# Performance work log

Hardware: AMD Instinct MI355X
Metric: run time of the kernel (lower is better)

Reference implementation:

```python
import jax, jax.numpy as jnp
import numpy as np

SEQ, BATCH, D, N = 256, 4, 512, 32768
TEMP = 0.5


def setup_inputs() -> dict:
    key = jax.random.key(0)
    ks = jax.random.split(key, 16)
    d = D
    # xavier_uniform with gain 1/sqrt(2) for square [d,d]: limit = gain*sqrt(6/(d+d))
    lim_t = (1.0 / np.sqrt(2.0)) * np.sqrt(6.0 / (d + d))
    lim_g1 = np.sqrt(6.0 / (2 * d + d))  # default kaiming-ish scale approximated by xavier
    lim_g2 = np.sqrt(6.0 / (d + 1))
    inp = {
        "q": jax.random.normal(ks[0], (SEQ, BATCH, D), dtype=jnp.float32),
        "prev_layer_output": jax.random.normal(ks[1], (SEQ, BATCH, D), dtype=jnp.float32),
        "Wq": jax.random.uniform(ks[2], (D, D), jnp.float32, -lim_t, lim_t),
        "bq": jnp.zeros((D,), jnp.float32),
        "Wk": jax.random.uniform(ks[3], (D, D), jnp.float32, -lim_t, lim_t),
        "bk": jnp.zeros((D,), jnp.float32),
        "Wv": jax.random.uniform(ks[4], (D, D), jnp.float32, -lim_t, lim_t),
        "bv": jnp.zeros((D,), jnp.float32),
        "Wg1": jax.random.uniform(ks[5], (D, 2 * D), jnp.float32, -lim_g1, lim_g1),
        "bg1": jnp.zeros((D,), jnp.float32),
        "Wg2": jax.random.uniform(ks[6], (1, D), jnp.float32, -lim_g2, lim_g2),
        "bg2": jnp.zeros((1,), jnp.float32),
        "dstore_k": jax.random.normal(ks[7], (N, D), dtype=jnp.float32),
        "dstore_v": jax.random.normal(ks[8], (N, D), dtype=jnp.float32),
    }
    return inp


def reference(q, prev_layer_output, Wq, bq, Wk, bk, Wv, bv, Wg1, bg1, Wg2, bg2, dstore_k, dstore_v):
    # [S,B,D] -> [B,S,D]
    qb = jnp.transpose(q, (1, 0, 2))
    prevb = jnp.transpose(prev_layer_output, (1, 0, 2))
    # enable_tune projections
    _q = qb @ Wq.T + bq                      # [B,S,D]
    _k = dstore_k @ Wk.T + bk                # [N,D]
    _v = dstore_v @ Wv.T + bv                # [N,D]
    _q = _q * (D ** -0.5)
    # attention over datastore, temperature-scaled softmax
    logits = jnp.einsum("bsd,nd->bsn", _q, _k) / TEMP  # [B,S,N]
    w = jax.nn.softmax(logits, axis=-1)
    attn = jnp.einsum("bsn,nd->bsd", w, _v)            # [B,S,D]
    # gated residual fusion
    cat = jnp.concatenate([attn, prevb], axis=-1)      # [B,S,2D]
    h = jax.nn.relu(cat @ Wg1.T + bg1)                 # [B,S,D]
    sigma = jax.nn.sigmoid(h @ Wg2.T + bg2)            # [B,S,1]
    res = attn * sigma + prevb * (1.0 - sigma)
    return jnp.transpose(res, (1, 0, 2))               # [S,B,D]
```

## Files before the change

### kernel.cpp

```cpp
#include <hip/hip_runtime.h>
#include <hip/hip_bf16.h>
#include <cstdint>
#include <cstddef>


typedef unsigned short u16;
typedef u16    u16x8 __attribute__((ext_vector_type(8)));
typedef u16    u16x4 __attribute__((ext_vector_type(4)));
typedef __bf16 bf16x8 __attribute__((ext_vector_type(8)));
typedef float  f32x4 __attribute__((ext_vector_type(4)));

#define MFMA16(a, b, c) __builtin_amdgcn_mfma_f32_16x16x32_bf16( \
    __builtin_bit_cast(bf16x8, (a)), __builtin_bit_cast(bf16x8, (b)), (c), 0, 0, 0)

__device__ __forceinline__ u16 f2bf(float f) {
  unsigned u = __builtin_bit_cast(unsigned, f);
  u += 0x7fffu + ((u >> 16) & 1u);
  return (u16)(u >> 16);
}

__global__ __launch_bounds__(256) void prep_kfrag(const float* __restrict__ src,
                                                  u16* __restrict__ dst) {
  const int sub = blockIdx.x;
  const int t = threadIdx.x;
  const float* s0 = src + (size_t)sub * 32 * 512;
  u16* d0 = dst + (size_t)sub * 16384;
#pragma unroll
  for (int u = 0; u < 8; u++) {
    int ci = t + 256 * u;
    int nh = ci >> 10, ks = (ci >> 6) & 15, ln = ci & 63;
    int qd = ln >> 4, l15 = ln & 15;
    const float* sp = s0 + (size_t)(nh * 16 + l15) * 512 + ks * 32 + qd * 8;
    float4 a = *(const float4*)sp;
    float4 b = *(const float4*)(sp + 4);
    u16x8 o = {f2bf(a.x), f2bf(a.y), f2bf(a.z), f2bf(a.w),
               f2bf(b.x), f2bf(b.y), f2bf(b.z), f2bf(b.w)};
    *(u16x8*)(d0 + (size_t)ci * 8) = o;
  }
}

__global__ __launch_bounds__(256) void prep_vt(const float* __restrict__ v,
                                               u16* __restrict__ vt) {
  __shared__ u16 Lt[64 * 72];
  const int n0 = blockIdx.x * 64, d0 = blockIdx.y * 64;
  const int t = threadIdx.x;
  const int n = t >> 2, c4 = t & 3;
#pragma unroll
  for (int i = 0; i < 4; i++) {
    int col = (c4 + 4 * i) * 4;
    float4 x = *(const float4*)(v + (size_t)(n0 + n) * 512 + d0 + col);
    Lt[(col + 0) * 72 + n] = f2bf(x.x);
    Lt[(col + 1) * 72 + n] = f2bf(x.y);
    Lt[(col + 2) * 72 + n] = f2bf(x.z);
    Lt[(col + 3) * 72 + n] = f2bf(x.w);
  }
  __syncthreads();
#pragma unroll
  for (int u = 0; u < 2; u++) {
    int unit = t + 256 * u;
    int d = unit >> 3, un = unit & 7;
    *(u16x8*)(vt + (size_t)(d0 + d) * 32768 + n0 + un * 8) =
        *(const u16x8*)&Lt[d * 72 + un * 8];
  }
}

template <bool TRANSB, bool CONCAT, bool RELU, bool OUTBF16, bool ROWSCALE>
__global__ __launch_bounds__(256, 2) void gemm64(
    const float* __restrict__ A, const float* __restrict__ A2,
    const float* __restrict__ B, const float* __restrict__ bias,
    const float* __restrict__ lvec, float alpha, void* __restrict__ Cv,
    int M, int N, int K) {
  __shared__ u16 As[64 * 72];
  __shared__ u16 Bs[64 * 72];
  const int tid = threadIdx.x;
  const int w = tid >> 6, lane = tid & 63, quad = lane >> 4, l15 = lane & 15;
  const int m0 = blockIdx.y * 64, n0 = blockIdx.x * 64;
  const int arow = tid >> 2, ac4 = tid & 3;
  float rs = 1.0f;
  if (ROWSCALE) rs = 1.0f / lvec[m0 + arow];
  const f32x4 fzero = {0.f, 0.f, 0.f, 0.f};
  f32x4 acc[4];
#pragma unroll
  for (int i = 0; i < 4; i++) acc[i] = fzero;

  for (int k0 = 0; k0 < K; k0 += 64) {
    __syncthreads();
    {
      const float* src;
      if (CONCAT)
        src = (k0 < 512) ? (A + (size_t)(m0 + arow) * 512 + k0)
                         : (A2 + (size_t)(m0 + arow) * 512 + (k0 - 512));
      else
        src = A + (size_t)(m0 + arow) * K + k0;
#pragma unroll
      for (int i = 0; i < 4; i++) {
        int col = (ac4 + 4 * i) * 4;
        float4 x = *(const float4*)(src + col);
        if (ROWSCALE) { x.x *= rs; x.y *= rs; x.z *= rs; x.w *= rs; }
        u16x4 o = {f2bf(x.x), f2bf(x.y), f2bf(x.z), f2bf(x.w)};
        *(u16x4*)&As[arow * 72 + col] = o;
      }
    }
    if (TRANSB) {
      const float* src = B + (size_t)(n0 + arow) * K + k0;
#pragma unroll
      for (int i = 0; i < 4; i++) {
        int col = (ac4 + 4 * i) * 4;
        float4 x = *(const float4*)(src + col);
        u16x4 o = {f2bf(x.x), f2bf(x.y), f2bf(x.z), f2bf(x.w)};
        *(u16x4*)&Bs[arow * 72 + col] = o;
      }
    } else {
      const float* src = B + (size_t)(k0 + arow) * N + n0;
#pragma unroll
      for (int i = 0; i < 4; i++) {
        int col = (ac4 + 4 * i) * 4;
        float4 x = *(const float4*)(src + col);
        Bs[(col + 0) * 72 + arow] = f2bf(x.x);
        Bs[(col + 1) * 72 + arow] = f2bf(x.y);
        Bs[(col + 2) * 72 + arow] = f2bf(x.z);
        Bs[(col + 3) * 72 + arow] = f2bf(x.w);
      }
    }
    __syncthreads();
#pragma unroll
    for (int ks = 0; ks < 2; ks++) {
      u16x8 af = *(const u16x8*)&As[(w * 16 + l15) * 72 + ks * 32 + quad * 8];
#pragma unroll
      for (int nt = 0; nt < 4; nt++) {
        u16x8 bf = *(const u16x8*)&Bs[(nt * 16 + l15) * 72 + ks * 32 + quad * 8];
        acc[nt] = MFMA16(af, bf, acc[nt]);
      }
    }
  }
#pragma unroll
  for (int nt = 0; nt < 4; nt++) {
    int col = n0 + nt * 16 + l15;
    float b = bias ? bias[col] : 0.f;
#pragma unroll
    for (int i = 0; i < 4; i++) {
      int row = m0 + w * 16 + quad * 4 + i;
      float y = (acc[nt][i] + b) * alpha;
      if (RELU) y = fmaxf(y, 0.f);
      if (OUTBF16)
        ((u16*)Cv)[(size_t)row * N + col] = f2bf(y);
      else
        ((float*)Cv)[(size_t)row * N + col] = y;
    }
  }
}

__global__ void cq_kernel(const float* __restrict__ q1,
                          const float* __restrict__ bk,
                          float* __restrict__ cq) {
  int r = blockIdx.x, lane = threadIdx.x;
  float s = 0.f;
#pragma unroll
  for (int k = 0; k < 512; k += 64) s += q1[(size_t)r * 512 + k + lane] * bk[k + lane];
#pragma unroll
  for (int off = 32; off; off >>= 1) s += __shfl_down(s, off, 64);
  if (lane == 0) cq[r] = 2.0f * s;
}

__global__ __launch_bounds__(512, 2) void flash(
    const u16* __restrict__ kfr,
    const u16* __restrict__ vt,
    const u16* __restrict__ q2,
    const float* __restrict__ cq,
    float* __restrict__ racc,
    float* __restrict__ lacc) {
  __shared__ u16 Es[2][64 * 40];
  const int tid = threadIdx.x;
  const int w = tid >> 6, lane = tid & 63, quad = lane >> 4, l15 = lane & 15;
  const int x = blockIdx.x & 7, j = blockIdx.x >> 3;
  const int ch = 2 * x + (j & 1), qt = j >> 1;
  const int qbase = qt * 64;
  const int qg = w >> 1, nh = w & 1;
  const int colb = w * 64;

  u16x8 qf[16];
  {
    const u16* qp = q2 + (size_t)(qbase + qg * 16 + l15) * 512 + quad * 8;
#pragma unroll
    for (int ks = 0; ks < 16; ks++) qf[ks] = *(const u16x8*)(qp + ks * 32);
  }
  float cq4[4];
#pragma unroll
  for (int i = 0; i < 4; i++) cq4[i] = cq[qbase + qg * 16 + quad * 4 + i];
  float lp[4] = {0.f, 0.f, 0.f, 0.f};
  const f32x4 fzero = {0.f, 0.f, 0.f, 0.f};
  f32x4 acc[4][4];
#pragma unroll
  for (int a = 0; a < 4; a++)
#pragma unroll
    for (int b = 0; b < 4; b++) acc[a][b] = fzero;

  const u16* kp0 = kfr + (((size_t)(ch * 64) * 2 + nh) * 16) * 512 + lane * 8;
  const u16* vp0 = vt + (size_t)(colb + l15) * 32768 + ch * 2048 + quad * 8;

  u16x8 kf[16];
  u16x8 bv[4];

#define LOAD_KF(SUB)                                                     \
  {                                                                      \
    const u16* kps = kp0 + (size_t)(SUB) * 16384;                        \
    _Pragma("unroll") for (int ks = 0; ks < 16; ks++)                    \
        kf[ks] = *(const u16x8*)(kps + ks * 512);                        \
  }
#define LOAD_V(SUB)                                                      \
  {                                                                      \
    _Pragma("unroll") for (int ct = 0; ct < 4; ct++)                     \
        bv[ct] = *(const u16x8*)(vp0 + (size_t)ct * (16 * 32768) +       \
                                 (SUB) * 32);                            \
  }
#define LOGITS(SV)                                                       \
  {                                                                      \
    f32x4 s0_ = fzero, s1_ = fzero;                                      \
    _Pragma("unroll") for (int ks = 0; ks < 16; ks += 2) {               \
      s0_ = MFMA16(qf[ks], kf[ks], s0_);                                 \
      s1_ = MFMA16(qf[ks + 1], kf[ks + 1], s1_);                         \
    }                                                                    \
    SV = s0_ + s1_;                                                      \
  }
#define PV_STEP(ER)                                                      \
  {                                                                      \
    u16x8 ef[4];                                                         \
    _Pragma("unroll") for (int q2i = 0; q2i < 4; q2i++)                  \
      ef[q2i] = *(const u16x8*)&(ER)[(q2i * 16 + l15) * 40 + quad * 8];  \
    _Pragma("unroll") for (int ct = 0; ct < 4; ct++)                     \
      _Pragma("unroll") for (int q2i = 0; q2i < 4; q2i++)                \
        acc[q2i][ct] = MFMA16(ef[q2i], bv[ct], acc[q2i][ct]);            \
  }
#define EXPW(EW, SV)                                                     \
  {                                                                      \
    _Pragma("unroll") for (int i = 0; i < 4; i++) {                      \
      float e = __expf(SV[i] + cq4[i]);                                  \
      lp[i] += e;                                                        \
      (EW)[(qg * 16 + quad * 4 + i) * 40 + nh * 16 + l15] = f2bf(e);     \
    }                                                                    \
  }
#define BARRIER()                                                        \
  {                                                                      \
    asm volatile("s_waitcnt lgkmcnt(0)" ::: "memory");                   \
    __builtin_amdgcn_s_barrier();                                        \
    __builtin_amdgcn_sched_barrier(0);                                   \
  }

  LOAD_KF(0);
  LOAD_V(0);
  {
    f32x4 s;
    LOGITS(s);
    EXPW(Es[0], s);
  }

#pragma unroll 1
  for (int sub = 1; sub < 64; ++sub) {
    BARRIER();
    LOAD_KF(sub);
    __builtin_amdgcn_s_setprio(1);
    PV_STEP(Es[(sub - 1) & 1]);
    __builtin_amdgcn_s_setprio(0);
    LOAD_V(sub);
    f32x4 s;
    LOGITS(s);
    EXPW(Es[sub & 1], s);
  }

  BARRIER();
  PV_STEP(Es[1]);

#undef LOAD_KF
#undef LOAD_V
#undef LOGITS
#undef PV_STEP
#undef EXPW
#undef BARRIER

#pragma unroll
  for (int q2i = 0; q2i < 4; q2i++)
#pragma unroll
    for (int ct = 0; ct < 4; ct++) {
      int col = colb + ct * 16 + l15;
#pragma unroll
      for (int i = 0; i < 4; i++) {
        int row = qbase + q2i * 16 + quad * 4 + i;
        atomicAdd(&racc[(size_t)row * 512 + col], acc[q2i][ct][i]);
      }
    }
#pragma unroll
  for (int i = 0; i < 4; i++) {
    float v = lp[i];
#pragma unroll
    for (int off = 1; off < 16; off <<= 1) v += __shfl_xor(v, off, 64);
    if (l15 == 0) atomicAdd(&lacc[qbase + qg * 16 + quad * 4 + i], v);
  }
}

__global__ __launch_bounds__(256) void finalize(
    const float* __restrict__ h, const float* __restrict__ attn,
    const float* __restrict__ prev, const float* __restrict__ wg2,
    const float* __restrict__ bg2, float* __restrict__ out) {
  __shared__ float red[4];
  int r = blockIdx.x, t = threadIdx.x;
  const float* hr = h + (size_t)r * 512;
  float p = hr[t] * wg2[t] + hr[t + 256] * wg2[t + 256];
#pragma unroll
  for (int off = 32; off; off >>= 1) p += __shfl_down(p, off, 64);
  if ((t & 63) == 0) red[t >> 6] = p;
  __syncthreads();
  float dot = red[0] + red[1] + red[2] + red[3];
  float sg = 1.f / (1.f + __expf(-(dot + bg2[0])));
  size_t base = (size_t)r * 512;
  out[base + t] = attn[base + t] * sg + prev[base + t] * (1.f - sg);
  out[base + t + 256] = attn[base + t + 256] * sg + prev[base + t + 256] * (1.f - sg);
}

extern "C" void kernel_launch(void* const* d_in, const int* in_sizes, int n_in,
                              void* d_out, int out_size, void* d_ws, size_t ws_size,
                              hipStream_t stream) {
  const float* q    = (const float*)d_in[0];
  const float* prev = (const float*)d_in[1];
  const float* Wq   = (const float*)d_in[2];
  const float* bq   = (const float*)d_in[3];
  const float* Wk   = (const float*)d_in[4];
  const float* bk   = (const float*)d_in[5];
  const float* Wv   = (const float*)d_in[6];
  const float* bv   = (const float*)d_in[7];
  const float* Wg1  = (const float*)d_in[8];
  const float* bg1  = (const float*)d_in[9];
  const float* Wg2  = (const float*)d_in[10];
  const float* bg2  = (const float*)d_in[11];
  const float* dk   = (const float*)d_in[12];
  const float* dv   = (const float*)d_in[13];
  float* out = (float*)d_out;

  char* ws = (char*)d_ws;
  u16*   kfr  = (u16*)(ws);
  u16*   vt   = (u16*)(ws + 33554432);
  float* racc = (float*)(ws + 67108864);
  float* lacc = (float*)(ws + 69206016);
  float* cqv  = (float*)(ws + 69210112);
  u16*   q2   = (u16*)(ws + 69214208);
  float* q1   = (float*)(ws + 70262784);
  float* attn = (float*)(ws + 72359936);
  float* h    = q1;

  prep_kfrag<<<1024, 256, 0, stream>>>(dk, kfr);
  prep_vt<<<dim3(512, 8), 256, 0, stream>>>(dv, vt);
  gemm64<true, false, false, false, false><<<dim3(8, 16), 256, 0, stream>>>(
      q, nullptr, Wq, bq, nullptr, 0.044194173824159216f, q1, 1024, 512, 512);
  cq_kernel<<<1024, 64, 0, stream>>>(q1, bk, cqv);
  gemm64<false, false, false, true, false><<<dim3(8, 16), 256, 0, stream>>>(
      q1, nullptr, Wk, nullptr, nullptr, 2.0f, q2, 1024, 512, 512);
  hipMemsetAsync(racc, 0, 2097152 + 4096, stream);
  flash<<<256, 512, 0, stream>>>(kfr, vt, q2, cqv, racc, lacc);
  gemm64<true, false, false, false, true><<<dim3(8, 16), 256, 0, stream>>>(
      racc, nullptr, Wv, bv, lacc, 1.0f, attn, 1024, 512, 512);
  gemm64<true, true, true, false, false><<<dim3(8, 16), 256, 0, stream>>>(
      attn, prev, Wg1, bg1, nullptr, 1.0f, h, 1024, 512, 1024);
  finalize<<<1024, 256, 0, stream>>>(h, attn, prev, Wg2, bg2, out);
}
```

Measured before the change: 431.3 us.

## Stage K fragments through LDS with async global_load_lds double buffering

K fragments are now copied straight into a double-buffered LDS tile with global_load_lds, one slice per wave, instead of each wave loading its full K fragment into registers. Each K tile is fetched once per block and shared by the wave pairs that read it. The loop is unrolled by two with ping-pong V register buffers, and the barriers now wait on vmcnt, so the next tile's loads overlap the current PV and logits MFMAs. The cost is 64KB more LDS per block, which may limit occupancy under launch_bounds(512,2), plus extra LDS reads in the logits step.

```diff
diff --git a/kernel.cpp b/kernel.cpp
--- a/kernel.cpp
+++ b/kernel.cpp
@@ -17,6 +17,12 @@
   unsigned u = __builtin_bit_cast(unsigned, f);
   u += 0x7fffu + ((u >> 16) & 1u);
   return (u16)(u >> 16);
+}
+
+__device__ __forceinline__ void glds16(const u16* g, u16* l) {
+  __builtin_amdgcn_global_load_lds(
+      (const __attribute__((address_space(1))) unsigned*)g,
+      (__attribute__((address_space(3))) unsigned*)l, 16, 0, 0);
 }
 
 __global__ __launch_bounds__(256) void prep_kfrag(const float* __restrict__ src,
@@ -169,7 +175,8 @@
     const float* __restrict__ cq,
     float* __restrict__ racc,
     float* __restrict__ lacc) {
-  __shared__ u16 Es[2][64 * 40];
+  __shared__ __align__(16) u16 Kb[2][16384];
+  __shared__ __align__(16) u16 Es[2][64 * 40];
   const int tid = threadIdx.x;
   const int w = tid >> 6, lane = tid & 63, quad = lane >> 4, l15 = lane & 15;
   const int x = blockIdx.x & 7, j = blockIdx.x >> 3;
@@ -195,41 +202,43 @@
 #pragma unroll
     for (int b = 0; b < 4; b++) acc[a][b] = fzero;
 
-  const u16* kp0 = kfr + (((size_t)(ch * 64) * 2 + nh) * 16) * 512 + lane * 8;
+  const u16* kg0 = kfr + (size_t)(ch * 64) * 16384 + w * 2048 + lane * 8;
   const u16* vp0 = vt + (size_t)(colb + l15) * 32768 + ch * 2048 + quad * 8;
 
-  u16x8 kf[16];
-  u16x8 bv[4];
-
-#define LOAD_KF(SUB)                                                     \
-  {                                                                      \
-    const u16* kps = kp0 + (size_t)(SUB) * 16384;                        \
-    _Pragma("unroll") for (int ks = 0; ks < 16; ks++)                    \
-        kf[ks] = *(const u16x8*)(kps + ks * 512);                        \
-  }
-#define LOAD_V(SUB)                                                      \
+  u16x8 bvA[4], bvB[4];
+
+#define GLDS_K(SUB, BI)                                                  \
+  {                                                                      \
+    const u16* gb = kg0 + (size_t)(SUB) * 16384;                         \
+    _Pragma("unroll") for (int u = 0; u < 4; u++)                        \
+        glds16(gb + u * 512, &Kb[BI][w * 2048 + u * 512]);               \
+  }
+#define LOAD_V(BV, SUB)                                                  \
   {                                                                      \
     _Pragma("unroll") for (int ct = 0; ct < 4; ct++)                     \
-        bv[ct] = *(const u16x8*)(vp0 + (size_t)ct * (16 * 32768) +       \
+        BV[ct] = *(const u16x8*)(vp0 + (size_t)ct * (16 * 32768) +       \
                                  (SUB) * 32);                            \
   }
-#define LOGITS(SV)                                                       \
+#define LOGITS(BI, SV)                                                   \
   {                                                                      \
     f32x4 s0_ = fzero, s1_ = fzero;                                      \
+    const u16* kb_ = &Kb[BI][nh * 8192 + lane * 8];                      \
     _Pragma("unroll") for (int ks = 0; ks < 16; ks += 2) {               \
-      s0_ = MFMA16(qf[ks], kf[ks], s0_);                                 \
-      s1_ = MFMA16(qf[ks + 1], kf[ks + 1], s1_);                         \
+      u16x8 k0_ = *(const u16x8*)(kb_ + ks * 512);                       \
+      u16x8 k1_ = *(const u16x8*)(kb_ + (ks + 1) * 512);                 \
+      s0_ = MFMA16(qf[ks], k0_, s0_);                                    \
+      s1_ = MFMA16(qf[ks + 1], k1_, s1_);                                \
     }                                                                    \
     SV = s0_ + s1_;                                                      \
   }
-#define PV_STEP(ER)                                                      \
+#define PV_STEP(ER, BV)                                                  \
   {                                                                      \
     u16x8 ef[4];                                                         \
     _Pragma("unroll") for (int q2i = 0; q2i < 4; q2i++)                  \
       ef[q2i] = *(const u16x8*)&(ER)[(q2i * 16 + l15) * 40 + quad * 8];  \
     _Pragma("unroll") for (int ct = 0; ct < 4; ct++)                     \
       _Pragma("unroll") for (int q2i = 0; q2i < 4; q2i++)                \
-        acc[q2i][ct] = MFMA16(ef[q2i], bv[ct], acc[q2i][ct]);            \
+        acc[q2i][ct] = MFMA16(ef[q2i], BV[ct], acc[q2i][ct]);            \
   }
 #define EXPW(EW, SV)                                                     \
   {                                                                      \
@@ -239,43 +248,69 @@
       (EW)[(qg * 16 + quad * 4 + i) * 40 + nh * 16 + l15] = f2bf(e);     \
     }                                                                    \
   }
-#define BARRIER()                                                        \
-  {                                                                      \
-    asm volatile("s_waitcnt lgkmcnt(0)" ::: "memory");                   \
+#define WAIT_BAR(VN)                                                     \
+  {                                                                      \
+    asm volatile("s_waitcnt vmcnt(" #VN ") lgkmcnt(0)" ::: "memory");    \
     __builtin_amdgcn_s_barrier();                                        \
     __builtin_amdgcn_sched_barrier(0);                                   \
   }
 
-  LOAD_KF(0);
-  LOAD_V(0);
+  GLDS_K(0, 0);
+  GLDS_K(1, 1);
+  LOAD_V(bvA, 0);
+  asm volatile("s_waitcnt vmcnt(8)" ::: "memory");
+  __builtin_amdgcn_s_barrier();
+  __builtin_amdgcn_sched_barrier(0);
   {
     f32x4 s;
-    LOGITS(s);
+    LOGITS(0, s);
     EXPW(Es[0], s);
   }
 
 #pragma unroll 1
-  for (int sub = 1; sub < 64; ++sub) {
-    BARRIER();
-    LOAD_KF(sub);
+  for (int sb = 1; sb < 62; sb += 2) {
+    WAIT_BAR(0);
+    GLDS_K(sb + 1, 0);
+    LOAD_V(bvB, sb);
+    __builtin_amdgcn_sched_barrier(0);
     __builtin_amdgcn_s_setprio(1);
-    PV_STEP(Es[(sub - 1) & 1]);
+    f32x4 s;
+    PV_STEP(Es[0], bvA);
+    LOGITS(1, s);
     __builtin_amdgcn_s_setprio(0);
-    LOAD_V(sub);
+    EXPW(Es[1], s);
+    WAIT_BAR(0);
+    GLDS_K(sb + 2, 1);
+    LOAD_V(bvA, sb + 1);
+    __builtin_amdgcn_sched_barrier(0);
+    __builtin_amdgcn_s_setprio(1);
+    f32x4 t;
+    PV_STEP(Es[1], bvB);
+    LOGITS(0, t);
+    __builtin_amdgcn_s_setprio(0);
+    EXPW(Es[0], t);
+  }
+
+  WAIT_BAR(0);
+  LOAD_V(bvB, 63);
+  __builtin_amdgcn_sched_barrier(0);
+  {
+    __builtin_amdgcn_s_setprio(1);
     f32x4 s;
-    LOGITS(s);
-    EXPW(Es[sub & 1], s);
-  }
-
-  BARRIER();
-  PV_STEP(Es[1]);
-
-#undef LOAD_KF
+    PV_STEP(Es[0], bvA);
+    LOGITS(1, s);
+    __builtin_amdgcn_s_setprio(0);
+    EXPW(Es[1], s);
+  }
+  WAIT_BAR(0);
+  PV_STEP(Es[1], bvB);
+
+#undef GLDS_K
 #undef LOAD_V
 #undef LOGITS
 #undef PV_STEP
 #undef EXPW
-#undef BARRIER
+#undef WAIT_BAR
 
 #pragma unroll
   for (int q2i = 0; q2i < 4; q2i++)
```

New measurement: 430.3 us. About the same (-0.2%).

## Warp-specialize flash kernel: logits warps with LDS-staged Q/K, PV warps stream V

Applied to the files above, without the earlier changes.

Splits the flash kernel's eight waves into four logit waves and four PV waves. The logit waves stage Q and the K tiles in shared memory, using global_load_lds for K with a prefetch of the next tile. The PV waves accumulate exp-weights times V over 128 columns each, with the two groups meeting at ping-pong barriers. Query tiles shrink from 64 to 32 rows and the grid doubles to 512 blocks with a higher occupancy target. This is meant to overlap the exp/logit path with the PV MFMAs and cut register pressure, at the cost of more K reloads per query and twice the atomic output traffic.

```diff
diff --git a/kernel.cpp b/kernel.cpp
--- a/kernel.cpp
+++ b/kernel.cpp
@@ -17,6 +17,12 @@
   unsigned u = __builtin_bit_cast(unsigned, f);
   u += 0x7fffu + ((u >> 16) & 1u);
   return (u16)(u >> 16);
+}
+
+__device__ __forceinline__ void glds16(const u16* g, u16* l) {
+  __builtin_amdgcn_global_load_lds(
+      (const __attribute__((address_space(1))) unsigned*)g,
+      (__attribute__((address_space(3))) unsigned*)l, 16, 0, 0);
 }
 
 __global__ __launch_bounds__(256) void prep_kfrag(const float* __restrict__ src,
@@ -162,74 +168,71 @@
   if (lane == 0) cq[r] = 2.0f * s;
 }
 
-__global__ __launch_bounds__(512, 2) void flash(
+__global__ __launch_bounds__(512, 4) void flash(
     const u16* __restrict__ kfr,
     const u16* __restrict__ vt,
     const u16* __restrict__ q2,
     const float* __restrict__ cq,
     float* __restrict__ racc,
     float* __restrict__ lacc) {
-  __shared__ u16 Es[2][64 * 40];
+  __shared__ __align__(16) u16 Qs[16384];
+  __shared__ __align__(16) u16 Kb[16384];
+  __shared__ __align__(16) u16 Es[2][32 * 40];
   const int tid = threadIdx.x;
   const int w = tid >> 6, lane = tid & 63, quad = lane >> 4, l15 = lane & 15;
   const int x = blockIdx.x & 7, j = blockIdx.x >> 3;
   const int ch = 2 * x + (j & 1), qt = j >> 1;
-  const int qbase = qt * 64;
-  const int qg = w >> 1, nh = w & 1;
-  const int colb = w * 64;
-
-  u16x8 qf[16];
-  {
-    const u16* qp = q2 + (size_t)(qbase + qg * 16 + l15) * 512 + quad * 8;
-#pragma unroll
-    for (int ks = 0; ks < 16; ks++) qf[ks] = *(const u16x8*)(qp + ks * 32);
-  }
+  const int qbase = qt * 32, nbase = ch * 2048;
+  const bool isL = (w < 4);
+  const int qg = (w >> 1) & 1, nh = w & 1;
+  const int colb = (w & 3) * 128;
+  const f32x4 fzero = {0.f, 0.f, 0.f, 0.f};
+
+#pragma unroll
+  for (int u = 0; u < 4; u++) {
+    int ci = tid + 512 * u;
+    int g = ci >> 10, ks = (ci >> 6) & 15, ln = ci & 63;
+    u16x8 v = *(const u16x8*)(q2 + (size_t)(qbase + g * 16 + (ln & 15)) * 512 +
+                              ks * 32 + (ln >> 4) * 8);
+    *(u16x8*)&Qs[(size_t)ci * 8] = v;
+  }
+
   float cq4[4];
-#pragma unroll
-  for (int i = 0; i < 4; i++) cq4[i] = cq[qbase + qg * 16 + quad * 4 + i];
   float lp[4] = {0.f, 0.f, 0.f, 0.f};
-  const f32x4 fzero = {0.f, 0.f, 0.f, 0.f};
-  f32x4 acc[4][4];
-#pragma unroll
-  for (int a = 0; a < 4; a++)
-#pragma unroll
-    for (int b = 0; b < 4; b++) acc[a][b] = fzero;
-
-  const u16* kp0 = kfr + (((size_t)(ch * 64) * 2 + nh) * 16) * 512 + lane * 8;
-  const u16* vp0 = vt + (size_t)(colb + l15) * 32768 + ch * 2048 + quad * 8;
-
-  u16x8 kf[16];
+  if (isL) {
+#pragma unroll
+    for (int i = 0; i < 4; i++) cq4[i] = cq[qbase + qg * 16 + quad * 4 + i];
+  }
+  f32x4 acc[2][8];
+#pragma unroll
+  for (int a = 0; a < 2; a++)
+#pragma unroll
+    for (int b = 0; b < 8; b++) acc[a][b] = fzero;
   u16x8 bv[4];
 
-#define LOAD_KF(SUB)                                                     \
-  {                                                                      \
-    const u16* kps = kp0 + (size_t)(SUB) * 16384;                        \
-    _Pragma("unroll") for (int ks = 0; ks < 16; ks++)                    \
-        kf[ks] = *(const u16x8*)(kps + ks * 512);                        \
-  }
-#define LOAD_V(SUB)                                                      \
-  {                                                                      \
-    _Pragma("unroll") for (int ct = 0; ct < 4; ct++)                     \
-        bv[ct] = *(const u16x8*)(vp0 + (size_t)ct * (16 * 32768) +       \
-                                 (SUB) * 32);                            \
+  const u16* kgb = kfr + (size_t)(ch * 64) * 16384 + w * 4096 + lane * 8;
+  const u16* vpb = vt + (size_t)(colb + l15) * 32768 + nbase + quad * 8;
+
+#define GLDS_K(R)                                                        \
+  {                                                                      \
+    const u16* gb = kgb + (size_t)(R) * 16384;                           \
+    _Pragma("unroll") for (int u = 0; u < 8; u++)                        \
+        glds16(gb + u * 512, &Kb[w * 4096 + u * 512]);                   \
   }
 #define LOGITS(SV)                                                       \
   {                                                                      \
     f32x4 s0_ = fzero, s1_ = fzero;                                      \
+    const u16* qb_ = &Qs[(qg * 16) * 512 + lane * 8];                    \
+    const u16* kb_ = &Kb[(nh * 16) * 512 + lane * 8];                    \
     _Pragma("unroll") for (int ks = 0; ks < 16; ks += 2) {               \
-      s0_ = MFMA16(qf[ks], kf[ks], s0_);                                 \
-      s1_ = MFMA16(qf[ks + 1], kf[ks + 1], s1_);                         \
+      u16x8 q0_ = *(const u16x8*)(qb_ + ks * 512);                       \
+      u16x8 k0_ = *(const u16x8*)(kb_ + ks * 512);                       \
+      u16x8 q1_ = *(const u16x8*)(qb_ + (ks + 1) * 512);                 \
+      u16x8 k1_ = *(const u16x8*)(kb_ + (ks + 1) * 512);                 \
+      s0_ = MFMA16(q0_, k0_, s0_);                                       \
+      s1_ = MFMA16(q1_, k1_, s1_);                                       \
     }                                                                    \
     SV = s0_ + s1_;                                                      \
-  }
-#define PV_STEP(ER)                                                      \
-  {                                                                      \
-    u16x8 ef[4];                                                         \
-    _Pragma("unroll") for (int q2i = 0; q2i < 4; q2i++)                  \
-      ef[q2i] = *(const u16x8*)&(ER)[(q2i * 16 + l15) * 40 + quad * 8];  \
-    _Pragma("unroll") for (int ct = 0; ct < 4; ct++)                     \
-      _Pragma("unroll") for (int q2i = 0; q2i < 4; q2i++)                \
-        acc[q2i][ct] = MFMA16(ef[q2i], bv[ct], acc[q2i][ct]);            \
   }
 #define EXPW(EW, SV)                                                     \
   {                                                                      \
@@ -239,62 +242,130 @@
       (EW)[(qg * 16 + quad * 4 + i) * 40 + nh * 16 + l15] = f2bf(e);     \
     }                                                                    \
   }
-#define BARRIER()                                                        \
-  {                                                                      \
+#define PV_PHASE(R, EPREV)                                               \
+  {                                                                      \
+    u16x8 ef0 = *(const u16x8*)&(EPREV)[l15 * 40 + quad * 8];            \
+    u16x8 ef1 = *(const u16x8*)&(EPREV)[(16 + l15) * 40 + quad * 8];     \
+    __builtin_amdgcn_s_setprio(1);                                       \
+    _Pragma("unroll") for (int ct = 0; ct < 4; ct++) {                   \
+      acc[0][ct] = MFMA16(ef0, bv[ct], acc[0][ct]);                      \
+      acc[1][ct] = MFMA16(ef1, bv[ct], acc[1][ct]);                      \
+    }                                                                    \
+    __builtin_amdgcn_s_setprio(0);                                       \
+    _Pragma("unroll") for (int ct = 0; ct < 4; ct++)                     \
+      bv[ct] = *(const u16x8*)(vpb + (size_t)(ct + 4) * (16 * 32768) +   \
+                               (size_t)(R - 1) * 32);                    \
+    __builtin_amdgcn_s_setprio(1);                                       \
+    _Pragma("unroll") for (int ct = 0; ct < 4; ct++) {                   \
+      acc[0][ct + 4] = MFMA16(ef0, bv[ct], acc[0][ct + 4]);              \
+      acc[1][ct + 4] = MFMA16(ef1, bv[ct], acc[1][ct + 4]);              \
+    }                                                                    \
+    __builtin_amdgcn_s_setprio(0);                                       \
+    _Pragma("unroll") for (int ct = 0; ct < 4; ct++)                     \
+      bv[ct] = *(const u16x8*)(vpb + (size_t)ct * (16 * 32768) +         \
+                               (size_t)(R) * 32);                        \
+  }
+#define BAR1()                                                           \
+  {                                                                      \
+    if (isL) asm volatile("s_waitcnt vmcnt(0)" ::: "memory");            \
     asm volatile("s_waitcnt lgkmcnt(0)" ::: "memory");                   \
     __builtin_amdgcn_s_barrier();                                        \
     __builtin_amdgcn_sched_barrier(0);                                   \
   }
-
-  LOAD_KF(0);
-  LOAD_V(0);
-  {
-    f32x4 s;
-    LOGITS(s);
-    EXPW(Es[0], s);
+#define BAR2()                                                           \
+  {                                                                      \
+    asm volatile("s_waitcnt lgkmcnt(0)" ::: "memory");                   \
+    __builtin_amdgcn_s_barrier();                                        \
+    __builtin_amdgcn_sched_barrier(0);                                   \
+  }
+#define REGION(R, PAR, IK)                                               \
+  {                                                                      \
+    BAR1();                                                              \
+    if (isL) {                                                           \
+      f32x4 sv_;                                                         \
+      __builtin_amdgcn_s_setprio(1);                                     \
+      LOGITS(sv_);                                                       \
+      __builtin_amdgcn_s_setprio(0);                                     \
+      BAR2();                                                            \
+      if (IK) GLDS_K((R) + 1);                                           \
+      EXPW(Es[PAR], sv_);                                                \
+    } else {                                                             \
+      PV_PHASE((R), Es[(PAR) ^ 1]);                                      \
+      BAR2();                                                            \
+    }                                                                    \
+  }
+
+  if (isL) GLDS_K(0);
+  BAR1();
+
+  if (isL) {
+    f32x4 sv_;
+    __builtin_amdgcn_s_setprio(1);
+    LOGITS(sv_);
+    __builtin_amdgcn_s_setprio(0);
+    BAR2();
+    GLDS_K(1);
+    EXPW(Es[0], sv_);
+  } else {
+#pragma unroll
+    for (int ct = 0; ct < 4; ct++)
+      bv[ct] = *(const u16x8*)(vpb + (size_t)ct * (16 * 32768));
+    BAR2();
   }
 
 #pragma unroll 1
-  for (int sub = 1; sub < 64; ++sub) {
-    BARRIER();
-    LOAD_KF(sub);
-    __builtin_amdgcn_s_setprio(1);
-    PV_STEP(Es[(sub - 1) & 1]);
-    __builtin_amdgcn_s_setprio(0);
-    LOAD_V(sub);
-    f32x4 s;
-    LOGITS(s);
-    EXPW(Es[sub & 1], s);
-  }
-
-  BARRIER();
-  PV_STEP(Es[1]);
-
-#undef LOAD_KF
-#undef LOAD_V
+  for (int r = 1; r < 63; r += 2) {
+    REGION(r, 1, 1);
+    REGION(r + 1, 0, 1);
+  }
+  REGION(63, 1, 0);
+
+  BAR1();
+  if (!isL) {
+    u16x8 ef0 = *(const u16x8*)&Es[1][l15 * 40 + quad * 8];
+    u16x8 ef1 = *(const u16x8*)&Es[1][(16 + l15) * 40 + quad * 8];
+#pragma unroll
+    for (int ct = 0; ct < 4; ct++) {
+      acc[0][ct] = MFMA16(ef0, bv[ct], acc[0][ct]);
+      acc[1][ct] = MFMA16(ef1, bv[ct], acc[1][ct]);
+    }
+#pragma unroll
+    for (int ct = 0; ct < 4; ct++)
+      bv[ct] = *(const u16x8*)(vpb + (size_t)(ct + 4) * (16 * 32768) +
+                               (size_t)63 * 32);
+#pragma unroll
+    for (int ct = 0; ct < 4; ct++) {
+      acc[0][ct + 4] = MFMA16(ef0, bv[ct], acc[0][ct + 4]);
+      acc[1][ct + 4] = MFMA16(ef1, bv[ct], acc[1][ct + 4]);
+    }
+#pragma unroll
+    for (int q2i = 0; q2i < 2; q2i++)
+#pragma unroll
+      for (int ct = 0; ct < 8; ct++) {
+        int col = colb + ct * 16 + l15;
+#pragma unroll
+        for (int i = 0; i < 4; i++) {
+          int row = qbase + q2i * 16 + quad * 4 + i;
+          atomicAdd(&racc[(size_t)row * 512 + col], acc[q2i][ct][i]);
+        }
+      }
+  } else {
+#pragma unroll
+    for (int i = 0; i < 4; i++) {
+      float v = lp[i];
+#pragma unroll
+      for (int off = 1; off < 16; off <<= 1) v += __shfl_xor(v, off, 64);
+      if (l15 == 0) atomicAdd(&lacc[qbase + qg * 16 + quad * 4 + i], v);
+    }
+  }
+
+#undef GLDS_K
 #undef LOGITS
-#undef PV_STEP
 #undef EXPW
-#undef BARRIER
-
-#pragma unroll
-  for (int q2i = 0; q2i < 4; q2i++)
-#pragma unroll
-    for (int ct = 0; ct < 4; ct++) {
-      int col = colb + ct * 16 + l15;
-#pragma unroll
-      for (int i = 0; i < 4; i++) {
-        int row = qbase + q2i * 16 + quad * 4 + i;
-        atomicAdd(&racc[(size_t)row * 512 + col], acc[q2i][ct][i]);
-      }
-    }
-#pragma unroll
-  for (int i = 0; i < 4; i++) {
-    float v = lp[i];
-#pragma unroll
-    for (int off = 1; off < 16; off <<= 1) v += __shfl_xor(v, off, 64);
-    if (l15 == 0) atomicAdd(&lacc[qbase + qg * 16 + quad * 4 + i], v);
-  }
+#undef PV_PHASE
+#undef BAR1
+#undef BAR2
+#undef REGION
 }
 
 __global__ __launch_bounds__(256) void finalize(
@@ -354,7 +425,7 @@
   gemm64<false, false, false, true, false><<<dim3(8, 16), 256, 0, stream>>>(
       q1, nullptr, Wk, nullptr, nullptr, 2.0f, q2, 1024, 512, 512);
   hipMemsetAsync(racc, 0, 2097152 + 4096, stream);
-  flash<<<256, 512, 0, stream>>>(kfr, vt, q2, cqv, racc, lacc);
+  flash<<<512, 512, 0, stream>>>(kfr, vt, q2, cqv, racc, lacc);
   gemm64<true, false, false, false, true><<<dim3(8, 16), 256, 0, stream>>>(
       racc, nullptr, Wv, bv, lacc, 1.0f, attn, 1024, 512, 512);
   gemm64<true, true, true, false, false><<<dim3(8, 16), 256, 0, stream>>>(
```

Result: slower. 990.9 us (+129.7%).
